# Kernel tuning notes

Hardware: AMD Instinct MI355X
Metric: run time of the kernel (lower is better)

The kernel has to match this reference:

```python
import jax, jax.numpy as jnp
import numpy as np

B, T, C = 2, 2048, 1024
NH = 16
HS = C // NH            # 64
BD = max(HS // 4, 16)   # 16
HORIZON = 32


def _windows(t, delta):
    # t: [B, nh, T, d] -> [B, nh, T, delta, d]; window w at pos i maps to original index i-delta+1+w
    padded = jnp.pad(t, ((0, 0), (0, 0), (delta - 1, 0), (0, 0)))
    idx = jnp.arange(t.shape[2])[:, None] + jnp.arange(delta)[None, :]
    return padded[:, :, idx]


def setup_inputs() -> dict:
    key = jax.random.key(0)
    ks = jax.random.split(key, 16)
    s = 0.02
    inp = {
        "x": jax.random.normal(ks[0], (B, T, C), dtype=jnp.float32),
        # weights stored [in, out] (transposed vs torch Linear)
        "w_disp": jax.random.normal(ks[1], (C, NH * BD), dtype=jnp.float32) * s,
        "b_disp": jnp.zeros((NH * BD,), dtype=jnp.float32),
        "w_val": jax.random.normal(ks[2], (C, C), dtype=jnp.float32) * s,
        "b_val": jnp.zeros((C,), dtype=jnp.float32),
        "rel_pos_emb": jax.random.normal(ks[3], (HORIZON, BD), dtype=jnp.float32) * s,
        "w_state": jax.random.normal(ks[4], (BD, BD), dtype=jnp.float32) * s,
        "b_state": jnp.zeros((BD,), dtype=jnp.float32),
        "w_strain": jax.random.normal(ks[5], (BD, BD), dtype=jnp.float32) * s,
        "b_strain": jnp.zeros((BD,), dtype=jnp.float32),
        "w_state_i": jax.random.normal(ks[6], (BD, BD), dtype=jnp.float32) * s,
        "w_state_j": jax.random.normal(ks[7], (BD, BD), dtype=jnp.float32) * s,
        "w_pos": jax.random.normal(ks[8], (BD, BD), dtype=jnp.float32) * s,
        "w_bond_out": jax.random.normal(ks[9], (BD, 1), dtype=jnp.float32) * s,
        "b_bond_out": jnp.zeros((1,), dtype=jnp.float32),
        "w_damage": jax.random.normal(ks[10], (BD, BD), dtype=jnp.float32) * s,
        "b_damage": jnp.zeros((BD,), dtype=jnp.float32),
        "w_damage_out": jax.random.normal(ks[11], (BD, 1), dtype=jnp.float32) * s,
        "b_damage_out": jnp.full((1,), -3.0, dtype=jnp.float32),
        "w_cproj": jax.random.normal(ks[12], (C, C), dtype=jnp.float32) * s,
        "b_cproj": jnp.zeros((C,), dtype=jnp.float32),
    }
    return inp


def reference(x, w_disp, b_disp, w_val, b_val, rel_pos_emb, w_state, b_state,
              w_strain, b_strain, w_state_i, w_state_j, w_pos,
              w_bond_out, b_bond_out, w_damage, b_damage,
              w_damage_out, b_damage_out, w_cproj, b_cproj):
    Bx, Tx, Cx = x.shape
    delta = min(HORIZON, Tx)
    gelu = lambda v: jax.nn.gelu(v, approximate=False)

    disp = (x @ w_disp + b_disp).reshape(Bx, Tx, NH, BD).transpose(0, 2, 1, 3)   # [B,nh,T,bd]
    val = (x @ w_val + b_val).reshape(Bx, Tx, NH, HS).transpose(0, 2, 1, 3)      # [B,nh,T,hs]

    disp_win = _windows(disp, delta)    # [B,nh,T,delta,bd]
    val_win = _windows(val, delta)      # [B,nh,T,delta,hs]

    cmask = (jnp.arange(Tx)[:, None] - delta + 1 + jnp.arange(delta)[None, :]) >= 0  # [T,delta]
    cmask_f = cmask.astype(x.dtype)

    strain = disp_win - disp[:, :, :, None, :]                                   # [B,nh,T,delta,bd]
    strain_for_state = strain @ w_state + b_state
    valid_counts = jnp.clip(cmask_f.sum(axis=-1), 1.0)                           # [T]
    state = (strain_for_state * cmask_f[None, None, :, :, None]).sum(axis=3) \
            / valid_counts[None, None, :, None]                                  # [B,nh,T,bd]
    state_win = _windows(state, delta)                                           # [B,nh,T,delta,bd]

    rel_emb = rel_pos_emb[:delta]                                                # [delta,bd]
    bond_act = gelu(strain @ w_strain + b_strain
                    + state[:, :, :, None, :] @ w_state_i
                    + state_win @ w_state_j
                    + rel_emb @ w_pos)                                           # [B,nh,T,delta,bd]
    bond_logits = (bond_act @ w_bond_out)[..., 0] + b_bond_out[0]                # [B,nh,T,delta]

    damage_act = gelu(strain @ w_damage + b_damage)
    damage = jax.nn.sigmoid((damage_act @ w_damage_out)[..., 0] + b_damage_out[0])

    logits = bond_logits - damage * 10.0
    logits = jnp.where(cmask[None, None], logits, -jnp.inf)
    weights = jax.nn.softmax(logits, axis=-1)                                    # [B,nh,T,delta]

    out = jnp.einsum('bntd,bntde->bnte', weights, val_win)                       # [B,nh,T,hs]
    out = out.transpose(0, 2, 1, 3).reshape(Bx, Tx, Cx)
    return out @ w_cproj + b_cproj
```

## Files before the change

kernel.cpp:

```cpp
#include <hip/hip_runtime.h>
#include <hip/hip_bf16.h>
#include <math.h>

constexpr int B_ = 2, T_ = 2048, C_ = 1024, NH_ = 16, HS_ = 64, BD_ = 16, DELTA_ = 32;
constexpr int M_ = B_ * T_;

typedef __bf16 bf16_t;
typedef __bf16 bf16x8 __attribute__((ext_vector_type(8)));
typedef float  f32x4  __attribute__((ext_vector_type(4)));

__device__ __forceinline__ float frcp(float x)  { return __builtin_amdgcn_rcpf(x); }
__device__ __forceinline__ float fexp2(float x) { return __builtin_amdgcn_exp2f(x); }
__device__ __forceinline__ float rlane(float v, int l) {
    return __builtin_bit_cast(float, __builtin_amdgcn_readlane(__builtin_bit_cast(int, v), l));
}

__device__ __forceinline__ float gelu_f(float x) {
    const float x2  = x * x;
    const float arg = x * fmaf(0.10294321f, x2, 2.3022074f);
    const float e   = fexp2(arg);
    const float r   = frcp(e + 1.0f);
    return x - x * r;
}
constexpr float LOG2E = 1.4426950409f;

__global__ __launch_bounds__(256) void convert_bf16_kernel(
    const float* __restrict__ in, bf16_t* __restrict__ out, int n)
{
    const int i = (blockIdx.x * 256 + threadIdx.x) * 8;
    if (i >= n) return;
    const float4 v0 = *(const float4*)(in + i);
    const float4 v1 = *(const float4*)(in + i + 4);
    bf16x8 o;
    o[0] = (bf16_t)v0.x; o[1] = (bf16_t)v0.y; o[2] = (bf16_t)v0.z; o[3] = (bf16_t)v0.w;
    o[4] = (bf16_t)v1.x; o[5] = (bf16_t)v1.y; o[6] = (bf16_t)v1.z; o[7] = (bf16_t)v1.w;
    *(bf16x8*)(out + i) = o;
}

__global__ __launch_bounds__(256) void transpose3_kernel(
    const float* __restrict__ w_val, const float* __restrict__ w_cproj,
    const float* __restrict__ w_disp,
    bf16_t* __restrict__ wvT, bf16_t* __restrict__ wcT, bf16_t* __restrict__ wdT)
{
    const int z = blockIdx.z;
    const float* in; bf16_t* out; int K = 1024, N = 1024;
    if (z == 0)      { in = w_val;   out = wvT; }
    else if (z == 1) { in = w_cproj; out = wcT; }
    else             { in = w_disp;  out = wdT; N = 256; if (blockIdx.x >= 8) return; }

    __shared__ float tile[32][33];
    const int n0 = blockIdx.x * 32, k0 = blockIdx.y * 32;
    const int tx = threadIdx.x & 31, ty = threadIdx.x >> 5;
    #pragma unroll
    for (int i = 0; i < 4; ++i)
        tile[ty + 8 * i][tx] = in[(size_t)(k0 + ty + 8 * i) * N + n0 + tx];
    __syncthreads();
    #pragma unroll
    for (int i = 0; i < 4; ++i)
        out[(size_t)(n0 + ty + 8 * i) * K + k0 + tx] = (bf16_t)tile[tx][ty + 8 * i];
}

__device__ __forceinline__ void gload16(const void* g, void* l) {
    __builtin_amdgcn_global_load_lds(
        (__attribute__((address_space(1))) void*)(g),
        (__attribute__((address_space(3))) void*)(l), 16, 0, 0);
}

#define GBM 128
#define GBN 64
#define GBK 32

__device__ __forceinline__ void gemm_core(
    bf16_t (*Al)[GBM][GBK], bf16_t (*Bl)[GBN][GBK],
    const bf16_t* __restrict__ A, const bf16_t* __restrict__ Bt,
    const float* __restrict__ bias, float* __restrict__ C,
    int N, int K, int bm, int bn)
{
    const int tid  = threadIdx.x;
    const int lane = tid & 63;
    const int w    = tid >> 6;
    const int wr   = w >> 1, wc = w & 1;

    const int lrow = lane >> 2;
    const int lcol = (lane & 3) * 8;
    const bf16_t* Ag0 = A  + (size_t)(bm + w * 32 + lrow) * K + lcol;
    const bf16_t* Ag1 = Ag0 + (size_t)16 * K;
    const bf16_t* Bg  = Bt + (size_t)(bn + w * 16 + lrow) * K + lcol;

    f32x4 acc[4][2] = {};
    const int nt = K / GBK;
    int cur = 0;

    gload16(Ag0, &Al[0][w * 32][0]);
    gload16(Ag1, &Al[0][w * 32 + 16][0]);
    gload16(Bg,  &Bl[0][w * 16][0]);
    __syncthreads();

    for (int t = 0; t < nt; ++t) {
        if (t + 1 < nt) {
            const int k1 = (t + 1) * GBK;
            gload16(Ag0 + k1, &Al[cur ^ 1][w * 32][0]);
            gload16(Ag1 + k1, &Al[cur ^ 1][w * 32 + 16][0]);
            gload16(Bg  + k1, &Bl[cur ^ 1][w * 16][0]);
        }
        bf16x8 af[4], bfr[2];
        #pragma unroll
        for (int i = 0; i < 4; ++i)
            af[i] = *(const bf16x8*)&Al[cur][wr * 64 + i * 16 + (lane & 15)][(lane >> 4) * 8];
        #pragma unroll
        for (int j = 0; j < 2; ++j)
            bfr[j] = *(const bf16x8*)&Bl[cur][wc * 32 + j * 16 + (lane & 15)][(lane >> 4) * 8];
        #pragma unroll
        for (int i = 0; i < 4; ++i)
            #pragma unroll
            for (int j = 0; j < 2; ++j)
                acc[i][j] = __builtin_amdgcn_mfma_f32_16x16x32_bf16(af[i], bfr[j], acc[i][j], 0, 0, 0);
        __syncthreads();
        cur ^= 1;
    }

    #pragma unroll
    for (int i = 0; i < 4; ++i) {
        const int r0 = bm + wr * 64 + i * 16 + (lane >> 4) * 4;
        #pragma unroll
        for (int j = 0; j < 2; ++j) {
            const int c = bn + wc * 32 + j * 16 + (lane & 15);
            const float bv = bias[c];
            float* cp = C + (size_t)r0 * N + c;
            #pragma unroll
            for (int q = 0; q < 4; ++q)
                cp[(size_t)q * N] = acc[i][j][q] + bv;
        }
    }
}

__global__ __launch_bounds__(256) void gemm_bf16_db(
    const bf16_t* __restrict__ A, const bf16_t* __restrict__ Bt,
    const float* __restrict__ bias, float* __restrict__ C,
    int M, int N, int K)
{
    __shared__ __align__(16) bf16_t Al[2][GBM][GBK];
    __shared__ __align__(16) bf16_t Bl[2][GBN][GBK];
    const int gx  = gridDim.x;
    const int nwg = gx * gridDim.y;
    const int bid = blockIdx.y * gx + blockIdx.x;
    const int wid = (bid & 7) * (nwg >> 3) + (bid >> 3);
    const int bx  = wid % gx, by = wid / gx;
    gemm_core(Al, Bl, A, Bt, bias, C, N, K, by * GBM, bx * GBN);
}

__global__ __launch_bounds__(256) void gemm_dv_fused(
    const bf16_t* __restrict__ A,
    const bf16_t* __restrict__ wvT, const bf16_t* __restrict__ wdT,
    const float* __restrict__ b_val, const float* __restrict__ b_disp,
    float* __restrict__ val, float* __restrict__ disp)
{
    __shared__ __align__(16) bf16_t Al[2][GBM][GBK];
    __shared__ __align__(16) bf16_t Bl[2][GBN][GBK];
    const int gx  = 20;
    const int nwg = 640;
    const int bid = blockIdx.y * gx + blockIdx.x;
    const int wid = (bid & 7) * (nwg >> 3) + (bid >> 3);
    const int bx  = wid % gx, by = wid / gx;
    if (bx < 16)
        gemm_core(Al, Bl, A, wvT, b_val, val, 1024, 1024, by * GBM, bx * GBN);
    else
        gemm_core(Al, Bl, A, wdT, b_disp, disp, 256, 1024, by * GBM, (bx - 16) * GBN);
}

#define PCT 128
__global__ __launch_bounds__(256) void precomp_kernel(
    const float* __restrict__ disp,
    const float* __restrict__ w_state, const float* __restrict__ b_state,
    const float* __restrict__ w_strain, const float* __restrict__ b_strain,
    const float* __restrict__ w_state_i, const float* __restrict__ w_state_j,
    const float* __restrict__ w_damage,
    float* __restrict__ P1, float* __restrict__ Q1, float* __restrict__ P2)
{
    __shared__ float s_d[PCT + 31][20];
    __shared__ float s_mv[PCT][20];
    __shared__ float s_st[PCT][20];
    __shared__ float s_wst[16][16], s_wstr[16][16], s_wsi[16][16], s_wsj[16][16], s_wdmg[16][16];
    __shared__ float s_bst[16], s_bstr[16];

    const int bid = blockIdx.x;
    const int tile = bid & (T_ / PCT - 1);
    const int h    = (bid >> 4) & 15;
    const int b    = bid >> 8;
    const int t0   = tile * PCT;
    const int tid  = threadIdx.x;

    s_wst[tid >> 4][tid & 15]  = w_state[tid];
    s_wstr[tid >> 4][tid & 15] = w_strain[tid];
    s_wsi[tid >> 4][tid & 15]  = w_state_i[tid];
    s_wsj[tid >> 4][tid & 15]  = w_state_j[tid];
    s_wdmg[tid >> 4][tid & 15] = w_damage[tid];
    if (tid < 16) { s_bst[tid] = b_state[tid]; s_bstr[tid] = b_strain[tid]; }

    for (int it = tid; it < (PCT + 31) * 4; it += 256) {
        const int row = it >> 2, q = it & 3;
        int rg = t0 - 31 + row; if (rg < 0) rg = 0;
        *(float4*)&s_d[row][q * 4] =
            *(const float4*)(disp + (size_t)(b * T_ + rg) * 256 + h * 16 + q * 4);
    }
    __syncthreads();

    #pragma unroll
    for (int p = 0; p < 8; ++p) {
        const int it = p * 256 + tid;
        const int tl = it >> 4, e = it & 15;
        const int t = t0 + tl;
        const int dlo = max(0, 31 - t);
        float s = 0.0f;
        for (int d = dlo; d < 32; ++d) s += s_d[tl + d][e];
        s_mv[tl][e] = s * frcp((float)(32 - dlo)) - s_d[tl + 31][e];
    }
    __syncthreads();

    #pragma unroll
    for (int p = 0; p < 8; ++p) {
        const int it = p * 256 + tid;
        const int tl = it >> 4, e = it & 15;
        float a = s_bst[e];
        #pragma unroll
        for (int k = 0; k < 16; ++k) a += s_mv[tl][k] * s_wst[k][e];
        s_st[tl][e] = a;
    }
    __syncthreads();

    #pragma unroll
    for (int p = 0; p < 8; ++p) {
        const int it = p * 256 + tid;
        const int tl = it >> 4, e = it & 15;
        float d1 = 0.0f, p2 = 0.0f, sj = 0.0f, si = 0.0f;
        #pragma unroll
        for (int k = 0; k < 16; ++k) {
            const float dv = s_d[tl + 31][k];
            const float sv = s_st[tl][k];
            d1 += dv * s_wstr[k][e];
            p2 += dv * s_wdmg[k][e];
            sj += sv * s_wsj[k][e];
            si += sv * s_wsi[k][e];
        }
        const size_t o = (size_t)(b * T_ + t0 + tl) * 256 + h * 16 + e;
        P1[o] = d1 + sj;
        Q1[o] = s_bstr[e] + si - d1;
        P2[o] = p2;
    }
}

__global__ __launch_bounds__(256, 4) void attn_kernel(
    const float* __restrict__ P1, const float* __restrict__ Q1,
    const float* __restrict__ P2, const float* __restrict__ val,
    const float* __restrict__ rel_pos_emb, const float* __restrict__ w_pos,
    const float* __restrict__ w_bond_out, const float* __restrict__ b_bond_out,
    const float* __restrict__ b_damage,
    const float* __restrict__ w_damage_out, const float* __restrict__ b_damage_out,
    bf16_t* __restrict__ att)
{
    __shared__ float  sP1[95][20], sP2[95][20], sQ1[64][20];
    __shared__ bf16_t sVal[95][72];
    __shared__ float  s_relw[32][20];
    __shared__ float  s_wb[16], s_wd[16], s_bd[16];

    const int tid  = threadIdx.x;
    const int bid  = blockIdx.x;
    const int tile = bid & 31;
    const int h    = (bid >> 5) & 15;
    const int b    = bid >> 9;
    const int t0   = tile * 64;

    for (int it = tid; it < 95 * 4; it += 256) {
        const int row = it >> 2, q = it & 3;
        int rg = t0 - 31 + row; if (rg < 0) rg = 0;
        const size_t o = (size_t)(b * T_ + rg) * 256 + h * 16 + q * 4;
        *(float4*)&sP1[row][q * 4] = *(const float4*)(P1 + o);
        *(float4*)&sP2[row][q * 4] = *(const float4*)(P2 + o);
    }
    {
        const int row = tid >> 2, q = tid & 3;
        *(float4*)&sQ1[row][q * 4] =
            *(const float4*)(Q1 + (size_t)(b * T_ + t0 + row) * 256 + h * 16 + q * 4);
    }
    for (int it = tid; it < 95 * 8; it += 256) {
        const int row = it >> 3, c8 = (it & 7) * 8;
        int rg = t0 - 31 + row; if (rg < 0) rg = 0;
        const float* vp = val + (size_t)(b * T_ + rg) * 1024 + h * 64 + c8;
        const float4 va = *(const float4*)(vp);
        const float4 vb = *(const float4*)(vp + 4);
        bf16x8 o;
        o[0] = (bf16_t)va.x; o[1] = (bf16_t)va.y; o[2] = (bf16_t)va.z; o[3] = (bf16_t)va.w;
        o[4] = (bf16_t)vb.x; o[5] = (bf16_t)vb.y; o[6] = (bf16_t)vb.z; o[7] = (bf16_t)vb.w;
        *(bf16x8*)&sVal[row][c8] = o;
    }
    {
        for (int it = tid; it < 512; it += 256) {
            const int dd = it >> 4, ee = it & 15;
            float a = 0.0f;
            #pragma unroll
            for (int k = 0; k < 16; ++k) a += rel_pos_emb[dd * 16 + k] * w_pos[k * 16 + ee];
            s_relw[dd][ee] = a;
        }
        if (tid < 16) {
            s_wb[tid] = w_bond_out[tid];
            s_wd[tid] = w_damage_out[tid];
            s_bd[tid] = b_damage[tid];
        }
    }
    __syncthreads();

    const int lane = tid & 63;
    const int w    = tid >> 6;
    const int half = lane >> 5;
    const int d    = lane & 31;
    const float bb  = b_bond_out[0];
    const float bdo = b_damage_out[0];

    float wv[8];

    #pragma unroll
    for (int pp = 0; pp < 8; ++pp) {
        const int p  = (w << 3) + pp;
        const int tl = (p << 1) + half;
        const int i  = tl + d;
        const bool valid = (t0 - 31 + i) >= 0;

        float bacc = 0.0f, dacc = 0.0f;
        #pragma unroll
        for (int q = 0; q < 4; ++q) {
            const float4 q1  = *(const float4*)&sQ1[tl][q * 4];
            const float4 p2t = *(const float4*)&sP2[tl + 31][q * 4];
            const float4 p1r = *(const float4*)&sP1[i][q * 4];
            const float4 p2r = *(const float4*)&sP2[i][q * 4];
            const float4 rw  = *(const float4*)&s_relw[d][q * 4];
            bacc += gelu_f(p1r.x + q1.x + rw.x) * s_wb[4 * q + 0];
            bacc += gelu_f(p1r.y + q1.y + rw.y) * s_wb[4 * q + 1];
            bacc += gelu_f(p1r.z + q1.z + rw.z) * s_wb[4 * q + 2];
            bacc += gelu_f(p1r.w + q1.w + rw.w) * s_wb[4 * q + 3];
            dacc += gelu_f(p2r.x - p2t.x + s_bd[4 * q + 0]) * s_wd[4 * q + 0];
            dacc += gelu_f(p2r.y - p2t.y + s_bd[4 * q + 1]) * s_wd[4 * q + 1];
            dacc += gelu_f(p2r.z - p2t.z + s_bd[4 * q + 2]) * s_wd[4 * q + 2];
            dacc += gelu_f(p2r.w - p2t.w + s_bd[4 * q + 3]) * s_wd[4 * q + 3];
        }

        float logit = -INFINITY;
        if (valid) {
            const float damage = frcp(1.0f + fexp2(-LOG2E * (dacc + bdo)));
            logit = bacc + bb - 10.0f * damage;
        }
        float m = logit;
        #pragma unroll
        for (int off = 16; off; off >>= 1) m = fmaxf(m, __shfl_xor(m, off, 32));
        const float pe = valid ? fexp2(LOG2E * (logit - m)) : 0.0f;
        float ss = pe;
        #pragma unroll
        for (int off = 16; off; off >>= 1) ss += __shfl_xor(ss, off, 32);
        wv[pp] = pe * frcp(ss);
    }

    #pragma unroll
    for (int pp = 0; pp < 8; ++pp) {
        const int tl0 = (w << 4) + (pp << 1);
        float acc0 = 0.0f, acc1 = 0.0f;
        #pragma unroll
        for (int j = 0; j < 33; ++j) {
            const float v = (float)sVal[tl0 + j][lane];
            if (j < 32) acc0 += rlane(wv[pp], j) * v;
            if (j >= 1) acc1 += rlane(wv[pp], 31 + j) * v;
        }
        const size_t o = (size_t)(b * T_ + t0 + tl0) * 1024 + h * 64 + lane;
        att[o]        = (bf16_t)acc0;
        att[o + 1024] = (bf16_t)acc1;
    }
}

extern "C" void kernel_launch(void* const* d_in, const int* in_sizes, int n_in,
                              void* d_out, int out_size, void* d_ws, size_t ws_size,
                              hipStream_t stream)
{
    const float* x        = (const float*)d_in[0];
    const float* w_disp   = (const float*)d_in[1];
    const float* b_disp   = (const float*)d_in[2];
    const float* w_val    = (const float*)d_in[3];
    const float* b_val    = (const float*)d_in[4];
    const float* rel      = (const float*)d_in[5];
    const float* w_state  = (const float*)d_in[6];
    const float* b_state  = (const float*)d_in[7];
    const float* w_strain = (const float*)d_in[8];
    const float* b_strain = (const float*)d_in[9];
    const float* w_si     = (const float*)d_in[10];
    const float* w_sj     = (const float*)d_in[11];
    const float* w_pos    = (const float*)d_in[12];
    const float* w_bond   = (const float*)d_in[13];
    const float* b_bond   = (const float*)d_in[14];
    const float* w_dmg    = (const float*)d_in[15];
    const float* b_dmg    = (const float*)d_in[16];
    const float* w_dout   = (const float*)d_in[17];
    const float* b_dout   = (const float*)d_in[18];
    const float* w_cproj  = (const float*)d_in[19];
    const float* b_cproj  = (const float*)d_in[20];

    float* out = (float*)d_out;
    float* ws  = (float*)d_ws;

    const size_t R = (size_t)M_ * 256;
    float* disp = ws;
    float* P1   = ws + R;
    float* Q1   = ws + 2 * R;
    float* P2   = ws + 3 * R;
    float* val  = ws + 4 * R;
    bf16_t* xb   = (bf16_t*)(ws + 8 * R);
    bf16_t* attb = xb;
    bf16_t* wdT  = (bf16_t*)(ws + 10 * R);
    bf16_t* wvT  = wdT + (size_t)256 * 1024;
    bf16_t* wcT  = wvT + (size_t)1024 * 1024;

    convert_bf16_kernel<<<(M_ * C_) / (256 * 8), 256, 0, stream>>>(x, xb, M_ * C_);
    transpose3_kernel<<<dim3(32, 32, 3), 256, 0, stream>>>(w_val, w_cproj, w_disp, wvT, wcT, wdT);

    gemm_dv_fused<<<dim3(20, 32), 256, 0, stream>>>(xb, wvT, wdT, b_val, b_disp, val, disp);

    precomp_kernel<<<B_ * NH_ * (T_ / PCT), 256, 0, stream>>>(
        disp, w_state, b_state, w_strain, b_strain, w_si, w_sj, w_dmg, P1, Q1, P2);

    attn_kernel<<<B_ * NH_ * (T_ / 64), 256, 0, stream>>>(
        P1, Q1, P2, val, rel, w_pos, w_bond, b_bond, b_dmg, w_dout, b_dout, attb);

    gemm_bf16_db<<<dim3(C_ / GBN, M_ / GBM), 256, 0, stream>>>(attb, wcT, b_cproj, out, M_, C_, C_);
}
```

Baseline: 215.4 us.

## Emit value projection in bf16, deepen GEMM K-step, read values directly in attention

The fused value/displacement GEMM now writes the value projection as bf16 rather than fp32. The attention kernel reads it straight from global memory instead of staging a bf16 copy in LDS, which frees shared memory and allows raising the occupancy hint from 4 to 6. The GEMM core now stages 64 K-elements per barrier (two 32-wide subtiles) to halve the number of synchronisations. Attention also specialises the causal-mask path so only the first tile evaluates the validity checks. The trade-offs are more LDS per GEMM block and uncached, strided global reads of values repeated across the window in attention.

```diff
diff --git a/kernel.cpp b/kernel.cpp
--- a/kernel.cpp
+++ b/kernel.cpp
@@ -68,12 +68,12 @@
 
 #define GBM 128
 #define GBN 64
-#define GBK 32
-
+
+template<typename OutT>
 __device__ __forceinline__ void gemm_core(
-    bf16_t (*Al)[GBM][GBK], bf16_t (*Bl)[GBN][GBK],
+    bf16_t (*Al)[2][GBM][32], bf16_t (*Bl)[2][GBN][32],
     const bf16_t* __restrict__ A, const bf16_t* __restrict__ Bt,
-    const float* __restrict__ bias, float* __restrict__ C,
+    const float* __restrict__ bias, OutT* __restrict__ C,
     int N, int K, int bm, int bn)
 {
     const int tid  = threadIdx.x;
@@ -83,38 +83,42 @@
 
     const int lrow = lane >> 2;
     const int lcol = (lane & 3) * 8;
-    const bf16_t* Ag0 = A  + (size_t)(bm + w * 32 + lrow) * K + lcol;
-    const bf16_t* Ag1 = Ag0 + (size_t)16 * K;
-    const bf16_t* Bg  = Bt + (size_t)(bn + w * 16 + lrow) * K + lcol;
+    const bf16_t* Ab = A  + (size_t)(bm + w * 32 + lrow) * K + lcol;
+    const bf16_t* Bb = Bt + (size_t)(bn + w * 16 + lrow) * K + lcol;
+
+    auto STAGE = [&](int buf, int k0) {
+        gload16(Ab + k0,                    &Al[buf][0][w * 32][0]);
+        gload16(Ab + (size_t)16 * K + k0,   &Al[buf][0][w * 32 + 16][0]);
+        gload16(Ab + k0 + 32,               &Al[buf][1][w * 32][0]);
+        gload16(Ab + (size_t)16 * K + k0 + 32, &Al[buf][1][w * 32 + 16][0]);
+        gload16(Bb + k0,                    &Bl[buf][0][w * 16][0]);
+        gload16(Bb + k0 + 32,               &Bl[buf][1][w * 16][0]);
+    };
 
     f32x4 acc[4][2] = {};
-    const int nt = K / GBK;
+    const int nt = K / 64;
     int cur = 0;
 
-    gload16(Ag0, &Al[0][w * 32][0]);
-    gload16(Ag1, &Al[0][w * 32 + 16][0]);
-    gload16(Bg,  &Bl[0][w * 16][0]);
+    STAGE(0, 0);
     __syncthreads();
 
     for (int t = 0; t < nt; ++t) {
-        if (t + 1 < nt) {
-            const int k1 = (t + 1) * GBK;
-            gload16(Ag0 + k1, &Al[cur ^ 1][w * 32][0]);
-            gload16(Ag1 + k1, &Al[cur ^ 1][w * 32 + 16][0]);
-            gload16(Bg  + k1, &Bl[cur ^ 1][w * 16][0]);
-        }
-        bf16x8 af[4], bfr[2];
-        #pragma unroll
-        for (int i = 0; i < 4; ++i)
-            af[i] = *(const bf16x8*)&Al[cur][wr * 64 + i * 16 + (lane & 15)][(lane >> 4) * 8];
-        #pragma unroll
-        for (int j = 0; j < 2; ++j)
-            bfr[j] = *(const bf16x8*)&Bl[cur][wc * 32 + j * 16 + (lane & 15)][(lane >> 4) * 8];
-        #pragma unroll
-        for (int i = 0; i < 4; ++i)
+        if (t + 1 < nt) STAGE(cur ^ 1, (t + 1) * 64);
+        #pragma unroll
+        for (int kk = 0; kk < 2; ++kk) {
+            bf16x8 af[4], bfr[2];
+            #pragma unroll
+            for (int i = 0; i < 4; ++i)
+                af[i] = *(const bf16x8*)&Al[cur][kk][wr * 64 + i * 16 + (lane & 15)][(lane >> 4) * 8];
             #pragma unroll
             for (int j = 0; j < 2; ++j)
-                acc[i][j] = __builtin_amdgcn_mfma_f32_16x16x32_bf16(af[i], bfr[j], acc[i][j], 0, 0, 0);
+                bfr[j] = *(const bf16x8*)&Bl[cur][kk][wc * 32 + j * 16 + (lane & 15)][(lane >> 4) * 8];
+            #pragma unroll
+            for (int i = 0; i < 4; ++i)
+                #pragma unroll
+                for (int j = 0; j < 2; ++j)
+                    acc[i][j] = __builtin_amdgcn_mfma_f32_16x16x32_bf16(af[i], bfr[j], acc[i][j], 0, 0, 0);
+        }
         __syncthreads();
         cur ^= 1;
     }
@@ -126,46 +130,47 @@
         for (int j = 0; j < 2; ++j) {
             const int c = bn + wc * 32 + j * 16 + (lane & 15);
             const float bv = bias[c];
-            float* cp = C + (size_t)r0 * N + c;
+            OutT* cp = C + (size_t)r0 * N + c;
             #pragma unroll
             for (int q = 0; q < 4; ++q)
-                cp[(size_t)q * N] = acc[i][j][q] + bv;
-        }
-    }
-}
-
+                cp[(size_t)q * N] = (OutT)(acc[i][j][q] + bv);
+        }
+    }
+}
+
+template<typename OutT>
 __global__ __launch_bounds__(256) void gemm_bf16_db(
     const bf16_t* __restrict__ A, const bf16_t* __restrict__ Bt,
-    const float* __restrict__ bias, float* __restrict__ C,
+    const float* __restrict__ bias, OutT* __restrict__ C,
     int M, int N, int K)
 {
-    __shared__ __align__(16) bf16_t Al[2][GBM][GBK];
-    __shared__ __align__(16) bf16_t Bl[2][GBN][GBK];
+    __shared__ __align__(16) bf16_t Al[2][2][GBM][32];
+    __shared__ __align__(16) bf16_t Bl[2][2][GBN][32];
     const int gx  = gridDim.x;
     const int nwg = gx * gridDim.y;
     const int bid = blockIdx.y * gx + blockIdx.x;
     const int wid = (bid & 7) * (nwg >> 3) + (bid >> 3);
     const int bx  = wid % gx, by = wid / gx;
-    gemm_core(Al, Bl, A, Bt, bias, C, N, K, by * GBM, bx * GBN);
+    gemm_core<OutT>(Al, Bl, A, Bt, bias, C, N, K, by * GBM, bx * GBN);
 }
 
 __global__ __launch_bounds__(256) void gemm_dv_fused(
     const bf16_t* __restrict__ A,
     const bf16_t* __restrict__ wvT, const bf16_t* __restrict__ wdT,
     const float* __restrict__ b_val, const float* __restrict__ b_disp,
-    float* __restrict__ val, float* __restrict__ disp)
-{
-    __shared__ __align__(16) bf16_t Al[2][GBM][GBK];
-    __shared__ __align__(16) bf16_t Bl[2][GBN][GBK];
+    bf16_t* __restrict__ valb, float* __restrict__ disp)
+{
+    __shared__ __align__(16) bf16_t Al[2][2][GBM][32];
+    __shared__ __align__(16) bf16_t Bl[2][2][GBN][32];
     const int gx  = 20;
     const int nwg = 640;
     const int bid = blockIdx.y * gx + blockIdx.x;
     const int wid = (bid & 7) * (nwg >> 3) + (bid >> 3);
     const int bx  = wid % gx, by = wid / gx;
     if (bx < 16)
-        gemm_core(Al, Bl, A, wvT, b_val, val, 1024, 1024, by * GBM, bx * GBN);
+        gemm_core<bf16_t>(Al, Bl, A, wvT, b_val, valb, 1024, 1024, by * GBM, bx * GBN);
     else
-        gemm_core(Al, Bl, A, wdT, b_disp, disp, 256, 1024, by * GBM, (bx - 16) * GBN);
+        gemm_core<float>(Al, Bl, A, wdT, b_disp, disp, 256, 1024, by * GBM, (bx - 16) * GBN);
 }
 
 #define PCT 128
@@ -249,73 +254,16 @@
     }
 }
 
-__global__ __launch_bounds__(256, 4) void attn_kernel(
-    const float* __restrict__ P1, const float* __restrict__ Q1,
-    const float* __restrict__ P2, const float* __restrict__ val,
-    const float* __restrict__ rel_pos_emb, const float* __restrict__ w_pos,
-    const float* __restrict__ w_bond_out, const float* __restrict__ b_bond_out,
-    const float* __restrict__ b_damage,
-    const float* __restrict__ w_damage_out, const float* __restrict__ b_damage_out,
-    bf16_t* __restrict__ att)
-{
-    __shared__ float  sP1[95][20], sP2[95][20], sQ1[64][20];
-    __shared__ bf16_t sVal[95][72];
-    __shared__ float  s_relw[32][20];
-    __shared__ float  s_wb[16], s_wd[16], s_bd[16];
-
-    const int tid  = threadIdx.x;
-    const int bid  = blockIdx.x;
-    const int tile = bid & 31;
-    const int h    = (bid >> 5) & 15;
-    const int b    = bid >> 9;
-    const int t0   = tile * 64;
-
-    for (int it = tid; it < 95 * 4; it += 256) {
-        const int row = it >> 2, q = it & 3;
-        int rg = t0 - 31 + row; if (rg < 0) rg = 0;
-        const size_t o = (size_t)(b * T_ + rg) * 256 + h * 16 + q * 4;
-        *(float4*)&sP1[row][q * 4] = *(const float4*)(P1 + o);
-        *(float4*)&sP2[row][q * 4] = *(const float4*)(P2 + o);
-    }
-    {
-        const int row = tid >> 2, q = tid & 3;
-        *(float4*)&sQ1[row][q * 4] =
-            *(const float4*)(Q1 + (size_t)(b * T_ + t0 + row) * 256 + h * 16 + q * 4);
-    }
-    for (int it = tid; it < 95 * 8; it += 256) {
-        const int row = it >> 3, c8 = (it & 7) * 8;
-        int rg = t0 - 31 + row; if (rg < 0) rg = 0;
-        const float* vp = val + (size_t)(b * T_ + rg) * 1024 + h * 64 + c8;
-        const float4 va = *(const float4*)(vp);
-        const float4 vb = *(const float4*)(vp + 4);
-        bf16x8 o;
-        o[0] = (bf16_t)va.x; o[1] = (bf16_t)va.y; o[2] = (bf16_t)va.z; o[3] = (bf16_t)va.w;
-        o[4] = (bf16_t)vb.x; o[5] = (bf16_t)vb.y; o[6] = (bf16_t)vb.z; o[7] = (bf16_t)vb.w;
-        *(bf16x8*)&sVal[row][c8] = o;
-    }
-    {
-        for (int it = tid; it < 512; it += 256) {
-            const int dd = it >> 4, ee = it & 15;
-            float a = 0.0f;
-            #pragma unroll
-            for (int k = 0; k < 16; ++k) a += rel_pos_emb[dd * 16 + k] * w_pos[k * 16 + ee];
-            s_relw[dd][ee] = a;
-        }
-        if (tid < 16) {
-            s_wb[tid] = w_bond_out[tid];
-            s_wd[tid] = w_damage_out[tid];
-            s_bd[tid] = b_damage[tid];
-        }
-    }
-    __syncthreads();
-
-    const int lane = tid & 63;
-    const int w    = tid >> 6;
-    const int half = lane >> 5;
-    const int d    = lane & 31;
-    const float bb  = b_bond_out[0];
-    const float bdo = b_damage_out[0];
-
+template<bool MASKED>
+__device__ __forceinline__ void attn_body(
+    const float (&sP1)[95][20], const float (&sP2)[95][20],
+    const float (&sQ1)[64][20], const float (&s_relw)[32][20],
+    const float* s_wb, const float* s_wd, const float* s_bd,
+    int t0, int w, int lane, int half, int d,
+    float bb, float bdo,
+    const bf16_t* __restrict__ vbase,
+    bf16_t* __restrict__ obase)
+{
     float wv[8];
 
     #pragma unroll
@@ -323,7 +271,7 @@
         const int p  = (w << 3) + pp;
         const int tl = (p << 1) + half;
         const int i  = tl + d;
-        const bool valid = (t0 - 31 + i) >= 0;
+        const bool valid = MASKED ? ((t0 - 31 + i) >= 0) : true;
 
         float bacc = 0.0f, dacc = 0.0f;
         #pragma unroll
@@ -343,15 +291,16 @@
             dacc += gelu_f(p2r.w - p2t.w + s_bd[4 * q + 3]) * s_wd[4 * q + 3];
         }
 
-        float logit = -INFINITY;
-        if (valid) {
-            const float damage = frcp(1.0f + fexp2(-LOG2E * (dacc + bdo)));
-            logit = bacc + bb - 10.0f * damage;
-        }
+        float logit;
+        const float damage = frcp(1.0f + fexp2(-LOG2E * (dacc + bdo)));
+        logit = bacc + bb - 10.0f * damage;
+        if (MASKED && !valid) logit = -INFINITY;
+
         float m = logit;
         #pragma unroll
         for (int off = 16; off; off >>= 1) m = fmaxf(m, __shfl_xor(m, off, 32));
-        const float pe = valid ? fexp2(LOG2E * (logit - m)) : 0.0f;
+        float pe = fexp2(LOG2E * (logit - m));
+        if (MASKED && !valid) pe = 0.0f;
         float ss = pe;
         #pragma unroll
         for (int off = 16; off; off >>= 1) ss += __shfl_xor(ss, off, 32);
@@ -364,14 +313,81 @@
         float acc0 = 0.0f, acc1 = 0.0f;
         #pragma unroll
         for (int j = 0; j < 33; ++j) {
-            const float v = (float)sVal[tl0 + j][lane];
+            int row = t0 + tl0 - 31 + j;
+            if (MASKED) row = row < 0 ? 0 : row;
+            const float v = (float)vbase[(size_t)row * 1024];
             if (j < 32) acc0 += rlane(wv[pp], j) * v;
             if (j >= 1) acc1 += rlane(wv[pp], 31 + j) * v;
         }
-        const size_t o = (size_t)(b * T_ + t0 + tl0) * 1024 + h * 64 + lane;
-        att[o]        = (bf16_t)acc0;
-        att[o + 1024] = (bf16_t)acc1;
-    }
+        obase[(size_t)tl0 * 1024]       = (bf16_t)acc0;
+        obase[(size_t)(tl0 + 1) * 1024] = (bf16_t)acc1;
+    }
+}
+
+__global__ __launch_bounds__(256, 6) void attn_kernel(
+    const float* __restrict__ P1, const float* __restrict__ Q1,
+    const float* __restrict__ P2, const bf16_t* __restrict__ valb,
+    const float* __restrict__ rel_pos_emb, const float* __restrict__ w_pos,
+    const float* __restrict__ w_bond_out, const float* __restrict__ b_bond_out,
+    const float* __restrict__ b_damage,
+    const float* __restrict__ w_damage_out, const float* __restrict__ b_damage_out,
+    bf16_t* __restrict__ att)
+{
+    __shared__ float sP1[95][20], sP2[95][20], sQ1[64][20];
+    __shared__ float s_relw[32][20];
+    __shared__ float s_wb[16], s_wd[16], s_bd[16];
+
+    const int tid  = threadIdx.x;
+    const int bid  = blockIdx.x;
+    const int tile = bid & 31;
+    const int h    = (bid >> 5) & 15;
+    const int b    = bid >> 9;
+    const int t0   = tile * 64;
+
+    for (int it = tid; it < 95 * 4; it += 256) {
+        const int row = it >> 2, q = it & 3;
+        int rg = t0 - 31 + row; if (rg < 0) rg = 0;
+        const size_t o = (size_t)(b * T_ + rg) * 256 + h * 16 + q * 4;
+        *(float4*)&sP1[row][q * 4] = *(const float4*)(P1 + o);
+        *(float4*)&sP2[row][q * 4] = *(const float4*)(P2 + o);
+    }
+    {
+        const int row = tid >> 2, q = tid & 3;
+        *(float4*)&sQ1[row][q * 4] =
+            *(const float4*)(Q1 + (size_t)(b * T_ + t0 + row) * 256 + h * 16 + q * 4);
+    }
+    {
+        for (int it = tid; it < 512; it += 256) {
+            const int dd = it >> 4, ee = it & 15;
+            float a = 0.0f;
+            #pragma unroll
+            for (int k = 0; k < 16; ++k) a += rel_pos_emb[dd * 16 + k] * w_pos[k * 16 + ee];
+            s_relw[dd][ee] = a;
+        }
+        if (tid < 16) {
+            s_wb[tid] = w_bond_out[tid];
+            s_wd[tid] = w_damage_out[tid];
+            s_bd[tid] = b_damage[tid];
+        }
+    }
+    __syncthreads();
+
+    const int lane = tid & 63;
+    const int w    = tid >> 6;
+    const int half = lane >> 5;
+    const int d    = lane & 31;
+    const float bb  = b_bond_out[0];
+    const float bdo = b_damage_out[0];
+
+    const bf16_t* vbase = valb + (size_t)b * T_ * 1024 + h * 64 + lane;
+    bf16_t* obase = att + (size_t)(b * T_ + t0) * 1024 + h * 64 + lane;
+
+    if (tile != 0)
+        attn_body<false>(sP1, sP2, sQ1, s_relw, s_wb, s_wd, s_bd,
+                         t0, w, lane, half, d, bb, bdo, vbase, obase);
+    else
+        attn_body<true>(sP1, sP2, sQ1, s_relw, s_wb, s_wd, s_bd,
+                        t0, w, lane, half, d, bb, bdo, vbase, obase);
 }
 
 extern "C" void kernel_launch(void* const* d_in, const int* in_sizes, int n_in,
@@ -408,23 +424,23 @@
     float* P1   = ws + R;
     float* Q1   = ws + 2 * R;
     float* P2   = ws + 3 * R;
-    float* val  = ws + 4 * R;
-    bf16_t* xb   = (bf16_t*)(ws + 8 * R);
+    bf16_t* xb   = (bf16_t*)(ws + 4 * R);
     bf16_t* attb = xb;
-    bf16_t* wdT  = (bf16_t*)(ws + 10 * R);
+    bf16_t* wdT  = (bf16_t*)(ws + 6 * R);
     bf16_t* wvT  = wdT + (size_t)256 * 1024;
     bf16_t* wcT  = wvT + (size_t)1024 * 1024;
+    bf16_t* valb = (bf16_t*)(ws + 8 * R);
 
     convert_bf16_kernel<<<(M_ * C_) / (256 * 8), 256, 0, stream>>>(x, xb, M_ * C_);
     transpose3_kernel<<<dim3(32, 32, 3), 256, 0, stream>>>(w_val, w_cproj, w_disp, wvT, wcT, wdT);
 
-    gemm_dv_fused<<<dim3(20, 32), 256, 0, stream>>>(xb, wvT, wdT, b_val, b_disp, val, disp);
+    gemm_dv_fused<<<dim3(20, 32), 256, 0, stream>>>(xb, wvT, wdT, b_val, b_disp, valb, disp);
 
     precomp_kernel<<<B_ * NH_ * (T_ / PCT), 256, 0, stream>>>(
         disp, w_state, b_state, w_strain, b_strain, w_si, w_sj, w_dmg, P1, Q1, P2);
 
     attn_kernel<<<B_ * NH_ * (T_ / 64), 256, 0, stream>>>(
-        P1, Q1, P2, val, rel, w_pos, w_bond, b_bond, b_dmg, w_dout, b_dout, attb);
-
-    gemm_bf16_db<<<dim3(C_ / GBN, M_ / GBM), 256, 0, stream>>>(attb, wcT, b_cproj, out, M_, C_, C_);
-}
+        P1, Q1, P2, valb, rel, w_pos, w_bond, b_bond, b_dmg, w_dout, b_dout, attb);
+
+    gemm_bf16_db<float><<<dim3(C_ / GBN, M_ / GBM), 256, 0, stream>>>(attb, wcT, b_cproj, out, M_, C_, C_);
+}
```

Result: slower. 288.0 us (+33.7%).
